# Kernel optimization log

Hardware: AMD Instinct MI355X
Metric: run time of the kernel (lower is better)

## Reference

```python
import jax, jax.numpy as jnp
import numpy as np

C_IN, K_R, K_C, N_K = 32, 3, 3, 64
STRIDE = (1, 1)
PAD = (1, 1)


def setup_inputs() -> dict:
    key = jax.random.key(0)
    k1, k2, k3 = jax.random.split(key, 3)
    x = jax.random.normal(k1, (32, C_IN, 128, 128), dtype=jnp.float32)
    kernels = jax.random.normal(k2, (N_K, K_R * K_C * C_IN), dtype=jnp.float32) * 0.05
    bias = jax.random.normal(k3, (N_K, 1), dtype=jnp.float32) * 0.05
    return {"x": x, "kernels": kernels, "bias": bias}


def reference(x, kernels, bias):
    # kernels rows are [C, kr, kc] flattened (per-channel im2col blocks stacked
    # along dim 0 in the original unroll) -> OIHW conv weight.
    w = kernels.reshape(N_K, C_IN, K_R, K_C)
    out = jax.lax.conv_general_dilated(
        x, w,
        window_strides=STRIDE,
        padding=[(PAD[0], PAD[0]), (PAD[1], PAD[1])],
        dimension_numbers=("NCHW", "OIHW", "NCHW"),
    )
    # bias (K, 1) broadcast over all output positions
    return out + bias.reshape(1, N_K, 1, 1)
```

## Files before the change

### kernel.cpp

```cpp
#include <hip/hip_runtime.h>
#include <hip/hip_bf16.h>


typedef __attribute__((ext_vector_type(8))) short bf16x8;
typedef __attribute__((ext_vector_type(4))) float f32x4;

#define NB 32
#define CIN 32
#define HH 128
#define WW 128
#define NK 64
#define XROW (130 * 32)

__device__ __forceinline__ unsigned short f2bf(float f) {
    union { float f; unsigned int u; } v; v.f = f;
    unsigned int u = v.u;
    return (unsigned short)((u + 0x7FFFu + ((u >> 16) & 1u)) >> 16);
}

__device__ __forceinline__ int xel(int wi, int c) {
    return wi * 32 + ((((c >> 3) ^ ((wi >> 2) & 3)) << 3) | (c & 7));
}

__global__ void repack_w(const float* __restrict__ kern,
                         unsigned short* __restrict__ wfrag) {
    int u = blockIdx.x * 256 + threadIdx.x;
    int j = u & 7;
    int lane = (u >> 3) & 63;
    int tile = (u >> 9) & 3;
    int kidx = u >> 11;
    int ok = tile * 16 + (lane & 15);
    int c = ((lane >> 4) << 3) + j;
    wfrag[u] = f2bf(kern[ok * 288 + c * 9 + kidx]);
}

__global__ __launch_bounds__(512, 4) void conv3x3_mfma(
        const float* __restrict__ x, const unsigned short* __restrict__ wfrag,
        const float* __restrict__ bias, float* __restrict__ out) {
    __shared__ unsigned short lds_x[6 * XROW];

    const int tid = threadIdx.x;
    const int bx = blockIdx.x;
    const int hgroup = ((bx & 7) << 2) | (bx >> 3);
    const int h0 = hgroup * 4;
    const int n = blockIdx.y;
    const int lane = tid & 63;
    const int l16 = lane & 15;
    const int q = lane >> 4;
    const int wav = tid >> 6;
    const int hsel = wav >> 2;
    const int sub = wav & 3;
    const int ok_tile = (sub & 1) * 2;
    const int w_base = (sub >> 1) * 64;

    if (tid < 384) {
        int it = tid >> 6;
        int idx = tid & 63;
        int c = idx & 31;
        int wi = (idx < 32) ? 0 : 129;
        lds_x[it * XROW + xel(wi, c)] = 0;
    }

    const int c = (tid >> 5) * 2;
    const int wq = tid & 31;

    #pragma unroll
    for (int it = 0; it < 4; ++it) {
        const int r = h0 - 1 + it;
        const bool valid = (unsigned)r < HH;
        float4 va = {0.f, 0.f, 0.f, 0.f}, vb = {0.f, 0.f, 0.f, 0.f};
        if (valid) {
            const float* xrow = x + (((size_t)n * CIN + c) * HH + r) * WW;
            va = *((const float4*)xrow + wq);
            vb = *((const float4*)(xrow + (size_t)HH * WW) + wq);
        }
        unsigned short* lrow = lds_x + it * XROW;
        #pragma unroll
        for (int j = 0; j < 4; ++j) {
            int w = wq * 4 + j;
            __hip_bfloat162 h2 = __float22bfloat162_rn(
                make_float2((&va.x)[j], (&vb.x)[j]));
            *(unsigned int*)&lrow[xel(w + 1, c)] = *(unsigned int*)&h2;
        }
    }

    float4 p0a, p0b, p1a = {0.f,0.f,0.f,0.f}, p1b = {0.f,0.f,0.f,0.f};
    {
        const float* xr3 = x + (((size_t)n * CIN + c) * HH + (h0 + 3)) * WW;
        p0a = *((const float4*)xr3 + wq);
        p0b = *((const float4*)(xr3 + (size_t)HH * WW) + wq);
        if (h0 + 4 < HH) {
            const float* xr4 = x + (((size_t)n * CIN + c) * HH + (h0 + 4)) * WW;
            p1a = *((const float4*)xr4 + wq);
            p1b = *((const float4*)(xr4 + (size_t)HH * WW) + wq);
        }
    }
    __syncthreads();

    f32x4 acc0[2][4];
    #pragma unroll
    for (int mi = 0; mi < 2; ++mi)
        #pragma unroll
        for (int ni = 0; ni < 4; ++ni)
            acc0[mi][ni] = (f32x4){0.f, 0.f, 0.f, 0.f};

    #pragma unroll 1
    for (int kr = 0; kr < 3; ++kr) {
        const unsigned short* lrow = lds_x + (hsel + kr) * XROW;
        #pragma unroll
        for (int kc = 0; kc < 3; ++kc) {
            const int kidx = kr * 3 + kc;
            bf16x8 afr[2];
            #pragma unroll
            for (int mi = 0; mi < 2; ++mi)
                afr[mi] = *(const bf16x8*)
                    &wfrag[(size_t)(((kidx * 4) + ok_tile + mi) * 64 + lane) * 8];
            #pragma unroll
            for (int ni = 0; ni < 4; ++ni) {
                bf16x8 bfr = *(const bf16x8*)&lrow[xel(w_base + ni * 16 + l16 + kc, q * 8)];
                #pragma unroll
                for (int mi = 0; mi < 2; ++mi)
                    acc0[mi][ni] = __builtin_amdgcn_mfma_f32_16x16x32_bf16(
                        afr[mi], bfr, acc0[mi][ni], 0, 0, 0);
            }
        }
    }

    {
        unsigned short* l4 = lds_x + 4 * XROW;
        unsigned short* l5 = lds_x + 5 * XROW;
        #pragma unroll
        for (int j = 0; j < 4; ++j) {
            int w = wq * 4 + j;
            __hip_bfloat162 h2a = __float22bfloat162_rn(
                make_float2((&p0a.x)[j], (&p0b.x)[j]));
            *(unsigned int*)&l4[xel(w + 1, c)] = *(unsigned int*)&h2a;
            __hip_bfloat162 h2b = __float22bfloat162_rn(
                make_float2((&p1a.x)[j], (&p1b.x)[j]));
            *(unsigned int*)&l5[xel(w + 1, c)] = *(unsigned int*)&h2b;
        }
    }
    __syncthreads();

    {
        const int h = h0 + hsel;
        #pragma unroll
        for (int mi = 0; mi < 2; ++mi) {
            #pragma unroll
            for (int rg = 0; rg < 4; ++rg) {
                int ok = (sub & 1) * 32 + mi * 16 + q * 4 + rg;
                float bv = bias[ok];
                float* orow = out + (((size_t)n * NK + ok) * HH + h) * WW;
                #pragma unroll
                for (int ni = 0; ni < 4; ++ni)
                    orow[w_base + ni * 16 + l16] = acc0[mi][ni][rg] + bv;
            }
        }
    }

    f32x4 acc1[2][4];
    #pragma unroll
    for (int mi = 0; mi < 2; ++mi)
        #pragma unroll
        for (int ni = 0; ni < 4; ++ni)
            acc1[mi][ni] = (f32x4){0.f, 0.f, 0.f, 0.f};

    #pragma unroll 1
    for (int kr = 0; kr < 3; ++kr) {
        const unsigned short* lrow = lds_x + (2 + hsel + kr) * XROW;
        #pragma unroll
        for (int kc = 0; kc < 3; ++kc) {
            const int kidx = kr * 3 + kc;
            bf16x8 afr[2];
            #pragma unroll
            for (int mi = 0; mi < 2; ++mi)
                afr[mi] = *(const bf16x8*)
                    &wfrag[(size_t)(((kidx * 4) + ok_tile + mi) * 64 + lane) * 8];
            #pragma unroll
            for (int ni = 0; ni < 4; ++ni) {
                bf16x8 bfr = *(const bf16x8*)&lrow[xel(w_base + ni * 16 + l16 + kc, q * 8)];
                #pragma unroll
                for (int mi = 0; mi < 2; ++mi)
                    acc1[mi][ni] = __builtin_amdgcn_mfma_f32_16x16x32_bf16(
                        afr[mi], bfr, acc1[mi][ni], 0, 0, 0);
            }
        }
    }

    {
        const int h = h0 + 2 + hsel;
        #pragma unroll
        for (int mi = 0; mi < 2; ++mi) {
            #pragma unroll
            for (int rg = 0; rg < 4; ++rg) {
                int ok = (sub & 1) * 32 + mi * 16 + q * 4 + rg;
                float bv = bias[ok];
                float* orow = out + (((size_t)n * NK + ok) * HH + h) * WW;
                #pragma unroll
                for (int ni = 0; ni < 4; ++ni)
                    orow[w_base + ni * 16 + l16] = acc1[mi][ni][rg] + bv;
            }
        }
    }
}

extern "C" void kernel_launch(void* const* d_in, const int* in_sizes, int n_in,
                              void* d_out, int out_size, void* d_ws, size_t ws_size,
                              hipStream_t stream) {
    const float* x    = (const float*)d_in[0];
    const float* kern = (const float*)d_in[1];
    const float* bias = (const float*)d_in[2];
    float* out = (float*)d_out;
    unsigned short* wfrag = (unsigned short*)d_ws;

    repack_w<<<72, 256, 0, stream>>>(kern, wfrag);
    dim3 grid(32, NB);
    conv3x3_mfma<<<grid, 512, 0, stream>>>(x, wfrag, bias, out);
}
```

Measured before the change: 190.4 us.

## Process eight rows per block with rolling LDS ring buffer and vectorized stores

Each block now covers eight output rows instead of four, using a six-row LDS ring buffer that is refilled from register-prefetched global rows while MFMAs run on the current rows. This cuts the redundant halo-row loads and amortizes setup across more work. The MFMA operands are swapped so each lane holds four consecutive output columns, which allows float4 stores, and bias is loaded once into registers. The cost is half as many blocks in the grid, which lowers parallelism, plus extra barriers and higher register pressure from the prefetch buffers.

```diff
diff --git a/kernel.cpp b/kernel.cpp
--- a/kernel.cpp
+++ b/kernel.cpp
@@ -41,8 +41,8 @@
 
     const int tid = threadIdx.x;
     const int bx = blockIdx.x;
-    const int hgroup = ((bx & 7) << 2) | (bx >> 3);
-    const int h0 = hgroup * 4;
+    const int hgroup = ((bx & 7) << 1) | (bx >> 3);
+    const int h0 = hgroup * 8;
     const int n = blockIdx.y;
     const int lane = tid & 63;
     const int l16 = lane & 15;
@@ -50,8 +50,13 @@
     const int wav = tid >> 6;
     const int hsel = wav >> 2;
     const int sub = wav & 3;
-    const int ok_tile = (sub & 1) * 2;
+    const int ok_t = (sub & 1) * 2;
     const int w_base = (sub >> 1) * 64;
+
+    float bias_r[2];
+    #pragma unroll
+    for (int mi = 0; mi < 2; ++mi)
+        bias_r[mi] = bias[(ok_t + mi) * 16 + l16];
 
     if (tid < 384) {
         int it = tid >> 6;
@@ -63,142 +68,110 @@
 
     const int c = (tid >> 5) * 2;
     const int wq = tid & 31;
+    const float* xc0 = x + ((size_t)n * CIN + c) * HH * WW;
+    const float* xc1 = xc0 + (size_t)HH * WW;
 
     #pragma unroll
     for (int it = 0; it < 4; ++it) {
         const int r = h0 - 1 + it;
-        const bool valid = (unsigned)r < HH;
         float4 va = {0.f, 0.f, 0.f, 0.f}, vb = {0.f, 0.f, 0.f, 0.f};
-        if (valid) {
-            const float* xrow = x + (((size_t)n * CIN + c) * HH + r) * WW;
-            va = *((const float4*)xrow + wq);
-            vb = *((const float4*)(xrow + (size_t)HH * WW) + wq);
+        if ((unsigned)r < HH) {
+            va = *((const float4*)(xc0 + (size_t)r * WW) + wq);
+            vb = *((const float4*)(xc1 + (size_t)r * WW) + wq);
         }
         unsigned short* lrow = lds_x + it * XROW;
         #pragma unroll
         for (int j = 0; j < 4; ++j) {
-            int w = wq * 4 + j;
             __hip_bfloat162 h2 = __float22bfloat162_rn(
                 make_float2((&va.x)[j], (&vb.x)[j]));
-            *(unsigned int*)&lrow[xel(w + 1, c)] = *(unsigned int*)&h2;
+            *(unsigned int*)&lrow[xel(wq * 4 + j + 1, c)] = *(unsigned int*)&h2;
         }
     }
 
-    float4 p0a, p0b, p1a = {0.f,0.f,0.f,0.f}, p1b = {0.f,0.f,0.f,0.f};
-    {
-        const float* xr3 = x + (((size_t)n * CIN + c) * HH + (h0 + 3)) * WW;
-        p0a = *((const float4*)xr3 + wq);
-        p0b = *((const float4*)(xr3 + (size_t)HH * WW) + wq);
-        if (h0 + 4 < HH) {
-            const float* xr4 = x + (((size_t)n * CIN + c) * HH + (h0 + 4)) * WW;
-            p1a = *((const float4*)xr4 + wq);
-            p1b = *((const float4*)(xr4 + (size_t)HH * WW) + wq);
-        }
-    }
+    float4 pre[2][4];
+    pre[0][0] = *((const float4*)(xc0 + (size_t)(h0 + 3) * WW) + wq);
+    pre[0][1] = *((const float4*)(xc1 + (size_t)(h0 + 3) * WW) + wq);
+    pre[0][2] = *((const float4*)(xc0 + (size_t)(h0 + 4) * WW) + wq);
+    pre[0][3] = *((const float4*)(xc1 + (size_t)(h0 + 4) * WW) + wq);
+
     __syncthreads();
 
-    f32x4 acc0[2][4];
     #pragma unroll
-    for (int mi = 0; mi < 2; ++mi)
+    for (int s = 0; s < 4; ++s) {
+        if (s < 2) {
+            const int r0 = h0 + 2 * s + 5;
+            const int r1 = h0 + 2 * s + 6;
+            pre[(s + 1) & 1][0] = *((const float4*)(xc0 + (size_t)r0 * WW) + wq);
+            pre[(s + 1) & 1][1] = *((const float4*)(xc1 + (size_t)r0 * WW) + wq);
+            if (r1 < HH) {
+                pre[(s + 1) & 1][2] = *((const float4*)(xc0 + (size_t)r1 * WW) + wq);
+                pre[(s + 1) & 1][3] = *((const float4*)(xc1 + (size_t)r1 * WW) + wq);
+            } else {
+                pre[(s + 1) & 1][2] = (float4){0.f, 0.f, 0.f, 0.f};
+                pre[(s + 1) & 1][3] = (float4){0.f, 0.f, 0.f, 0.f};
+            }
+        }
+
+        f32x4 acc[2][4];
         #pragma unroll
-        for (int ni = 0; ni < 4; ++ni)
-            acc0[mi][ni] = (f32x4){0.f, 0.f, 0.f, 0.f};
+        for (int mi = 0; mi < 2; ++mi)
+            #pragma unroll
+            for (int wt = 0; wt < 4; ++wt)
+                acc[mi][wt] = (f32x4){0.f, 0.f, 0.f, 0.f};
 
-    #pragma unroll 1
-    for (int kr = 0; kr < 3; ++kr) {
-        const unsigned short* lrow = lds_x + (hsel + kr) * XROW;
-        #pragma unroll
-        for (int kc = 0; kc < 3; ++kc) {
-            const int kidx = kr * 3 + kc;
-            bf16x8 afr[2];
+        #pragma unroll 1
+        for (int kr = 0; kr < 3; ++kr) {
+            int bi = 2 * s + hsel + kr;
+            if (bi >= 6) bi -= 6;
+            const unsigned short* lrow = lds_x + bi * XROW;
             #pragma unroll
-            for (int mi = 0; mi < 2; ++mi)
-                afr[mi] = *(const bf16x8*)
-                    &wfrag[(size_t)(((kidx * 4) + ok_tile + mi) * 64 + lane) * 8];
-            #pragma unroll
-            for (int ni = 0; ni < 4; ++ni) {
-                bf16x8 bfr = *(const bf16x8*)&lrow[xel(w_base + ni * 16 + l16 + kc, q * 8)];
+            for (int kc = 0; kc < 3; ++kc) {
+                const int kidx = kr * 3 + kc;
+                bf16x8 wf[2];
                 #pragma unroll
                 for (int mi = 0; mi < 2; ++mi)
-                    acc0[mi][ni] = __builtin_amdgcn_mfma_f32_16x16x32_bf16(
-                        afr[mi], bfr, acc0[mi][ni], 0, 0, 0);
+                    wf[mi] = *(const bf16x8*)
+                        &wfrag[(size_t)(((kidx * 4) + ok_t + mi) * 64 + lane) * 8];
+                #pragma unroll
+                for (int wt = 0; wt < 4; ++wt) {
+                    bf16x8 xf = *(const bf16x8*)
+                        &lrow[xel(w_base + wt * 16 + l16 + kc, q * 8)];
+                    #pragma unroll
+                    for (int mi = 0; mi < 2; ++mi)
+                        acc[mi][wt] = __builtin_amdgcn_mfma_f32_16x16x32_bf16(
+                            xf, wf[mi], acc[mi][wt], 0, 0, 0);
+                }
             }
         }
-    }
 
-    {
-        unsigned short* l4 = lds_x + 4 * XROW;
-        unsigned short* l5 = lds_x + 5 * XROW;
-        #pragma unroll
-        for (int j = 0; j < 4; ++j) {
-            int w = wq * 4 + j;
-            __hip_bfloat162 h2a = __float22bfloat162_rn(
-                make_float2((&p0a.x)[j], (&p0b.x)[j]));
-            *(unsigned int*)&l4[xel(w + 1, c)] = *(unsigned int*)&h2a;
-            __hip_bfloat162 h2b = __float22bfloat162_rn(
-                make_float2((&p1a.x)[j], (&p1b.x)[j]));
-            *(unsigned int*)&l5[xel(w + 1, c)] = *(unsigned int*)&h2b;
+        if (s < 3) {
+            unsigned short* lr0 = lds_x + ((2 * s + 4) % 6) * XROW;
+            unsigned short* lr1 = lds_x + ((2 * s + 5) % 6) * XROW;
+            #pragma unroll
+            for (int j = 0; j < 4; ++j) {
+                __hip_bfloat162 h2a = __float22bfloat162_rn(
+                    make_float2((&pre[s & 1][0].x)[j], (&pre[s & 1][1].x)[j]));
+                *(unsigned int*)&lr0[xel(wq * 4 + j + 1, c)] = *(unsigned int*)&h2a;
+                __hip_bfloat162 h2b = __float22bfloat162_rn(
+                    make_float2((&pre[s & 1][2].x)[j], (&pre[s & 1][3].x)[j]));
+                *(unsigned int*)&lr1[xel(wq * 4 + j + 1, c)] = *(unsigned int*)&h2b;
+            }
+            __syncthreads();
         }
-    }
-    __syncthreads();
 
-    {
-        const int h = h0 + hsel;
-        #pragma unroll
-        for (int mi = 0; mi < 2; ++mi) {
+        {
+            const int h = h0 + 2 * s + hsel;
             #pragma unroll
-            for (int rg = 0; rg < 4; ++rg) {
-                int ok = (sub & 1) * 32 + mi * 16 + q * 4 + rg;
-                float bv = bias[ok];
+            for (int mi = 0; mi < 2; ++mi) {
+                const int ok = (ok_t + mi) * 16 + l16;
+                const float bv = bias_r[mi];
                 float* orow = out + (((size_t)n * NK + ok) * HH + h) * WW;
                 #pragma unroll
-                for (int ni = 0; ni < 4; ++ni)
-                    orow[w_base + ni * 16 + l16] = acc0[mi][ni][rg] + bv;
-            }
-        }
-    }
-
-    f32x4 acc1[2][4];
-    #pragma unroll
-    for (int mi = 0; mi < 2; ++mi)
-        #pragma unroll
-        for (int ni = 0; ni < 4; ++ni)
-            acc1[mi][ni] = (f32x4){0.f, 0.f, 0.f, 0.f};
-
-    #pragma unroll 1
-    for (int kr = 0; kr < 3; ++kr) {
-        const unsigned short* lrow = lds_x + (2 + hsel + kr) * XROW;
-        #pragma unroll
-        for (int kc = 0; kc < 3; ++kc) {
-            const int kidx = kr * 3 + kc;
-            bf16x8 afr[2];
-            #pragma unroll
-            for (int mi = 0; mi < 2; ++mi)
-                afr[mi] = *(const bf16x8*)
-                    &wfrag[(size_t)(((kidx * 4) + ok_tile + mi) * 64 + lane) * 8];
-            #pragma unroll
-            for (int ni = 0; ni < 4; ++ni) {
-                bf16x8 bfr = *(const bf16x8*)&lrow[xel(w_base + ni * 16 + l16 + kc, q * 8)];
-                #pragma unroll
-                for (int mi = 0; mi < 2; ++mi)
-                    acc1[mi][ni] = __builtin_amdgcn_mfma_f32_16x16x32_bf16(
-                        afr[mi], bfr, acc1[mi][ni], 0, 0, 0);
-            }
-        }
-    }
-
-    {
-        const int h = h0 + 2 + hsel;
-        #pragma unroll
-        for (int mi = 0; mi < 2; ++mi) {
-            #pragma unroll
-            for (int rg = 0; rg < 4; ++rg) {
-                int ok = (sub & 1) * 32 + mi * 16 + q * 4 + rg;
-                float bv = bias[ok];
-                float* orow = out + (((size_t)n * NK + ok) * HH + h) * WW;
-                #pragma unroll
-                for (int ni = 0; ni < 4; ++ni)
-                    orow[w_base + ni * 16 + l16] = acc1[mi][ni][rg] + bv;
+                for (int wt = 0; wt < 4; ++wt) {
+                    f32x4 v = acc[mi][wt];
+                    float4 o = make_float4(v[0] + bv, v[1] + bv, v[2] + bv, v[3] + bv);
+                    *(float4*)&orow[w_base + wt * 16 + q * 4] = o;
+                }
             }
         }
     }
@@ -214,6 +187,6 @@
     unsigned short* wfrag = (unsigned short*)d_ws;
 
     repack_w<<<72, 256, 0, stream>>>(kern, wfrag);
-    dim3 grid(32, NB);
+    dim3 grid(16, NB);
     conv3x3_mfma<<<grid, 512, 0, stream>>>(x, wfrag, bias, out);
 }
```

Result: slower. 219.1 us (+15.0%).
